# Kernel tuning notes

Hardware: AMD Instinct MI355X
Metric: run time of the kernel (lower is better)

The kernel has to match this reference:

```python
import jax, jax.numpy as jnp
import numpy as np

HIDDEN = 2048
HEADS = 16
HEAD_DIM = HIDDEN // HEADS


def setup_inputs() -> dict:
    key = jax.random.key(0)
    ks = jax.random.split(key, 5)
    scale = 1.0 / np.sqrt(HIDDEN)
    x = jax.random.normal(ks[0], (2, 2048, HIDDEN), dtype=jnp.float32)
    wq = jax.random.normal(ks[1], (HIDDEN, HIDDEN), dtype=jnp.float32) * scale
    wk = jax.random.normal(ks[2], (HIDDEN, HIDDEN), dtype=jnp.float32) * scale
    wv = jax.random.normal(ks[3], (HIDDEN, HIDDEN), dtype=jnp.float32) * scale
    wo = jax.random.normal(ks[4], (HIDDEN, HIDDEN), dtype=jnp.float32) * scale
    return {"x": x, "wq": wq, "wk": wk, "wv": wv, "wo": wo}


def reference(x, wq, wk, wv, wo):
    B, S, D = x.shape
    # nn.Linear(w, bias=False): y = x @ w.T
    q = (x @ wq.T).reshape(B, S, HEADS, HEAD_DIM)
    k = (x @ wk.T).reshape(B, S, HEADS, HEAD_DIM)
    v = (x @ wv.T).reshape(B, S, HEADS, HEAD_DIM)
    scores = jnp.einsum("bqhd,bkhd->bhqk", q, k) / jnp.sqrt(
        jnp.asarray(HEAD_DIM, dtype=x.dtype)
    )
    causal_mask = jnp.triu(jnp.ones((S, S), dtype=bool), k=1)
    scores = jnp.where(causal_mask, -jnp.inf, scores)
    attn = jax.nn.softmax(scores, axis=-1)
    out = jnp.einsum("bhqk,bkhd->bqhd", attn, v).reshape(B, S, D)
    return out @ wo.T
```

## Files before the change

kernel.cpp:

```cpp
#include <hip/hip_runtime.h>
#include <hip/hip_bf16.h>
#include <math.h>

typedef unsigned short u16;
typedef __attribute__((ext_vector_type(8))) short bf16x8;
typedef __attribute__((ext_vector_type(4))) float f32x4;

__device__ static inline u16 f2bf(float f) {
  unsigned u = __float_as_uint(f);
  u += 0x7fff + ((u >> 16) & 1);
  return (u16)(u >> 16);
}

__device__ static inline void gload_lds16(const void* g, void* l) {
  __builtin_amdgcn_global_load_lds(
      (const __attribute__((address_space(1))) unsigned int*)g,
      (__attribute__((address_space(3))) unsigned int*)l, 16, 0, 0);
}

__device__ static inline void store_out(u16* p, float v)   { *p = f2bf(v); }
__device__ static inline void store_out(float* p, float v) { *p = v; }

__global__ void cvt_f32_bf16(const float* __restrict__ src, u16* __restrict__ dst, int n) {
  int stride = gridDim.x * blockDim.x;
  for (int i = blockIdx.x * blockDim.x + threadIdx.x; i * 8 < n; i += stride) {
    const float4* s4 = (const float4*)(src + (size_t)i * 8);
    float4 a = s4[0], b = s4[1];
    u16 t[8] = { f2bf(a.x), f2bf(a.y), f2bf(a.z), f2bf(a.w),
                 f2bf(b.x), f2bf(b.y), f2bf(b.z), f2bf(b.w) };
    *(bf16x8*)(dst + (size_t)i * 8) = *(bf16x8*)t;
  }
}

__global__ void cvt3_f32_bf16(const float* __restrict__ s0, const float* __restrict__ s1,
                              const float* __restrict__ s2, u16* __restrict__ dst) {
  const float* s = blockIdx.y == 0 ? s0 : (blockIdx.y == 1 ? s1 : s2);
  size_t i = ((size_t)blockIdx.x * blockDim.x + threadIdx.x) * 8;
  const float4* s4 = (const float4*)(s + i);
  float4 a = s4[0], b = s4[1];
  u16 t[8] = { f2bf(a.x), f2bf(a.y), f2bf(a.z), f2bf(a.w),
               f2bf(b.x), f2bf(b.y), f2bf(b.z), f2bf(b.w) };
  *(bf16x8*)(dst + (size_t)blockIdx.y * 4194304 + i) = *(bf16x8*)t;
}

template <int NF, typename OutT>
__global__ __launch_bounds__(512, 2)
void gemm2ph(const u16* __restrict__ A, const u16* __restrict__ Bm,
             OutT* __restrict__ C, int M, int N, int K) {
  constexpr int BN = NF * 64;
  __shared__ u16 Abuf[2][256 * 64];
  __shared__ u16 Bbuf[2][BN * 64];
  const int tid = threadIdx.x, lane = tid & 63, w = tid >> 6;
  const int wm = w >> 2, wn = w & 3;
  const int g = lane >> 4, l16 = lane & 15;

  const int per = gridDim.x >> 3;
  const int swz = ((int)blockIdx.x & 7) * per + ((int)blockIdx.x >> 3);
  const int nx = N / BN;
  const int bx = swz % nx, by = swz / nx;
  const int brow = by << 8, bcol = bx * BN;
  const int nt = K >> 6;

  auto stage_Ah = [&](int h, int kt, int d) {
    char* lds = (char*)Abuf[d] + h * 16384;
#pragma unroll
    for (int i = 0; i < 2; ++i) {
      int idx = i * 512 + tid;
      int r = h * 128 + (idx >> 3);
      int c = ((idx & 7) * 16) ^ ((r & 7) << 4);
      gload_lds16((const char*)(A + (size_t)(brow + r) * K + kt * 64) + c,
                  lds + idx * 16);
    }
  };
  auto stage_B = [&](int kt, int d) {
    char* lds = (char*)Bbuf[d];
#pragma unroll
    for (int i = 0; i < NF; ++i) {
      int idx = i * 512 + tid;
      int r = idx >> 3;
      int c = ((idx & 7) * 16) ^ ((r & 7) << 4);
      gload_lds16((const char*)(Bm + (size_t)(bcol + r) * K + kt * 64) + c,
                  lds + idx * 16);
    }
  };

  f32x4 acc[8][NF] = {};
  bf16x8 afr[4][2], bfr[NF][2];

  auto lda = [&](int d, int mf0) {
#pragma unroll
    for (int mf = 0; mf < 4; ++mf) {
      int r = wm * 128 + (mf0 + mf) * 16 + l16;
      const char* base = (const char*)Abuf[d] + r * 128;
      int sw = (r & 7) << 4;
#pragma unroll
      for (int ks = 0; ks < 2; ++ks)
        afr[mf][ks] = *(const bf16x8*)(base + ((ks * 64 + g * 16) ^ sw));
    }
  };
  auto ldb = [&](int d) {
#pragma unroll
    for (int nf = 0; nf < NF; ++nf) {
      int r = wn * (NF * 16) + nf * 16 + l16;
      const char* base = (const char*)Bbuf[d] + r * 128;
      int sw = (r & 7) << 4;
#pragma unroll
      for (int ks = 0; ks < 2; ++ks)
        bfr[nf][ks] = *(const bf16x8*)(base + ((ks * 64 + g * 16) ^ sw));
    }
  };
  auto mma_half = [&](int mf0) {
    __builtin_amdgcn_s_setprio(1);
#pragma unroll
    for (int mf = 0; mf < 4; ++mf)
#pragma unroll
      for (int nf = 0; nf < NF; ++nf)
#pragma unroll
        for (int ks = 0; ks < 2; ++ks)
          acc[mf0 + mf][nf] = __builtin_amdgcn_mfma_f32_16x16x32_bf16(
              afr[mf][ks], bfr[nf][ks], acc[mf0 + mf][nf], 0, 0, 0);
    __builtin_amdgcn_s_setprio(0);
  };

#define WAIT_LGKM() do { \
    asm volatile("s_waitcnt lgkmcnt(0)" ::: "memory"); \
    __builtin_amdgcn_sched_barrier(0); } while (0)
#define WAIT_VM_NF() do { \
    if constexpr (NF == 3) asm volatile("s_waitcnt vmcnt(3)" ::: "memory"); \
    else                   asm volatile("s_waitcnt vmcnt(2)" ::: "memory"); \
    __builtin_amdgcn_sched_barrier(0); } while (0)

  stage_Ah(0, 0, 0); stage_Ah(1, 0, 0);
  stage_B(0, 0);
  stage_B(1, 1);
  WAIT_VM_NF();
  __builtin_amdgcn_s_barrier();

  for (int t = 0; t < nt; ++t) {
    const int cur = t & 1;
    lda(cur, 0); ldb(cur);
    if (t + 1 < nt) stage_Ah(0, t + 1, cur ^ 1);
    __builtin_amdgcn_s_barrier();
    WAIT_LGKM();
    mma_half(0);
    __builtin_amdgcn_s_barrier();
    lda(cur, 4);
    if (t + 1 < nt) stage_Ah(1, t + 1, cur ^ 1);
    if (t + 2 < nt) stage_B(t + 2, cur);
    __builtin_amdgcn_s_barrier();
    WAIT_LGKM();
    mma_half(4);
    if (t + 1 < nt) {
      if (t + 2 < nt) { WAIT_VM_NF(); }
      else {
        asm volatile("s_waitcnt vmcnt(0)" ::: "memory");
        __builtin_amdgcn_sched_barrier(0);
      }
      __builtin_amdgcn_s_barrier();
    }
  }
#undef WAIT_LGKM
#undef WAIT_VM_NF

  const size_t cb = (size_t)(brow + wm * 128) * N + bcol + wn * (NF * 16);
#pragma unroll
  for (int mf = 0; mf < 8; ++mf)
#pragma unroll
    for (int nf = 0; nf < NF; ++nf) {
      int col = nf * 16 + l16;
#pragma unroll
      for (int rr = 0; rr < 4; ++rr) {
        int row = mf * 16 + g * 4 + rr;
        store_out(C + cb + (size_t)row * N + col, acc[mf][nf][rr]);
      }
    }
}

__global__ __launch_bounds__(256)
void transpose_v(const u16* __restrict__ QKV, u16* __restrict__ Vt) {
  __shared__ u16 t[64][72];
  const int tid = threadIdx.x;
  const int b = blockIdx.y >> 5;
  const int s0 = (blockIdx.y & 31) * 64;
  const int hd0 = blockIdx.x * 64;
  const int lr = tid >> 2, lc = (tid & 3) * 16;
  const u16* src = QKV + ((size_t)(b * 2048 + s0 + lr) * 6144 + 4096 + hd0 + lc);
  *(bf16x8*)&t[lr][lc]     = *(const bf16x8*)src;
  *(bf16x8*)&t[lr][lc + 8] = *(const bf16x8*)(src + 8);
  __syncthreads();
  u16 tmp[16];
#pragma unroll
  for (int j = 0; j < 16; ++j) tmp[j] = t[lc + j][lr];
  u16* dst = Vt + ((size_t)(b * 2048 + hd0 + lr) * 2048 + s0 + lc);
  *(bf16x8*)dst       = *(bf16x8*)tmp;
  *(bf16x8*)(dst + 8) = *(bf16x8*)(tmp + 8);
}

__global__ __launch_bounds__(256, 2)
void attn_fwd(const u16* __restrict__ QKV, const u16* __restrict__ Vt,
              u16* __restrict__ AO) {
  __shared__ u16 Ks[2][64 * 128];
  __shared__ u16 Vs[2][128 * 64];
  __shared__ u16 Ps[4][16 * 64];
  const int tid = threadIdx.x, lane = tid & 63, w = tid >> 6;
  const int g = lane >> 4, l16 = lane & 15;
  const int bh = blockIdx.y, b = bh >> 4, h = bh & 15;
  const int fold = blockIdx.x;
  const int pswz = (l16 & 7) << 4;

  for (int phase = 0; phase < 2; ++phase) {
    const int qt = phase == 0 ? fold : 31 - fold;
    const int q0 = qt * 64 + w * 16;

    bf16x8 qf[4];
    {
      const u16* qrow = QKV + ((size_t)(b * 2048 + q0 + l16) * 6144 + h * 128 + g * 8);
#pragma unroll
      for (int c = 0; c < 4; ++c) qf[c] = *(const bf16x8*)(qrow + c * 32);
    }
    f32x4 o[8] = {};
    float mrun = -INFINITY, lrun = 0.f;

    auto stage = [&](int it, int d) {
      int kv0 = it * 64;
#pragma unroll
      for (int i = 0; i < 4; ++i) {
        int idx = i * 256 + tid;
        {
          int row = idx >> 4;
          int scolb = ((idx & 15) * 16) ^ ((row & 7) << 4);
          gload_lds16((const char*)QKV +
                          ((size_t)(b * 2048 + kv0 + row) * 6144 + 2048 + h * 128) * 2 + scolb,
                      (char*)Ks[d] + idx * 16);
        }
        {
          int dd = idx >> 3;
          int vcolb = ((idx & 7) * 16) ^ ((dd & 7) << 4);
          gload_lds16((const char*)Vt + ((size_t)(bh * 128 + dd) * 2048 + kv0) * 2 + vcolb,
                      (char*)Vs[d] + idx * 16);
        }
      }
    };

    const int ntkv = qt + 1;
    stage(0, 0);
    for (int it = 0; it < ntkv; ++it) {
      const int kv0 = it * 64, cur = it & 1;
      if (it + 1 < ntkv) {
        stage(it + 1, cur ^ 1);
        asm volatile("s_waitcnt vmcnt(8)" ::: "memory");
      } else {
        asm volatile("s_waitcnt vmcnt(0)" ::: "memory");
      }
      __builtin_amdgcn_sched_barrier(0);
      __builtin_amdgcn_s_barrier();

      f32x4 s[4];
#pragma unroll
      for (int kb = 0; kb < 4; ++kb) {
        if (kv0 + kb * 16 > q0 + 15) {
          s[kb] = f32x4{-INFINITY, -INFINITY, -INFINITY, -INFINITY};
          continue;
        }
        f32x4 a = {};
        int row = kb * 16 + l16;
        int swzk = (row & 7) << 4;
#pragma unroll
        for (int c = 0; c < 4; ++c) {
          bf16x8 kf = *(const bf16x8*)((const char*)Ks[cur] + row * 256 + ((c * 64 + g * 16) ^ swzk));
          a = __builtin_amdgcn_mfma_f32_16x16x32_bf16(kf, qf[c], a, 0, 0, 0);
        }
        s[kb] = a * 0.08838834764831845f;
      }
      if (kv0 == qt * 64) {
#pragma unroll
        for (int kb = 0; kb < 4; ++kb)
#pragma unroll
          for (int r = 0; r < 4; ++r)
            if (kv0 + kb * 16 + g * 4 + r > q0 + l16) s[kb][r] = -INFINITY;
      }

      float mloc = -INFINITY;
#pragma unroll
      for (int kb = 0; kb < 4; ++kb)
#pragma unroll
        for (int r = 0; r < 4; ++r) mloc = fmaxf(mloc, s[kb][r]);
      mloc = fmaxf(mloc, __shfl_xor(mloc, 16));
      mloc = fmaxf(mloc, __shfl_xor(mloc, 32));
      float mnew = fmaxf(mrun, mloc);
      float al = __expf(mrun - mnew);
      mrun = mnew;
      float rsum = 0.f;
#pragma unroll
      for (int kb = 0; kb < 4; ++kb) {
        float p0 = __expf(s[kb][0] - mnew);
        float p1 = __expf(s[kb][1] - mnew);
        float p2 = __expf(s[kb][2] - mnew);
        float p3 = __expf(s[kb][3] - mnew);
        rsum += (p0 + p1) + (p2 + p3);
        ushort4 pk = { f2bf(p0), f2bf(p1), f2bf(p2), f2bf(p3) };
        *(ushort4*)((char*)Ps[w] + l16 * 128 + ((kb * 32 + g * 8) ^ pswz)) = pk;
      }
      rsum += __shfl_xor(rsum, 16);
      rsum += __shfl_xor(rsum, 32);
      lrun = lrun * al + rsum;

      float alq[4];
#pragma unroll
      for (int r = 0; r < 4; ++r) alq[r] = __shfl(al, g * 4 + r);
#pragma unroll
      for (int db = 0; db < 8; ++db)
#pragma unroll
        for (int r = 0; r < 4; ++r) o[db][r] *= alq[r];

#pragma unroll
      for (int ks = 0; ks < 2; ++ks) {
        if (kv0 + ks * 32 > q0 + 15) continue;
        bf16x8 pa = *(const bf16x8*)((const char*)Ps[w] + l16 * 128 + ((ks * 64 + g * 16) ^ pswz));
#pragma unroll
        for (int db = 0; db < 8; ++db) {
          int row = db * 16 + l16;
          int swzv = (row & 7) << 4;
          bf16x8 vf = *(const bf16x8*)((const char*)Vs[cur] + row * 128 + ((ks * 64 + g * 16) ^ swzv));
          o[db] = __builtin_amdgcn_mfma_f32_16x16x32_bf16(pa, vf, o[db], 0, 0, 0);
        }
      }
      __builtin_amdgcn_s_barrier();
    }

    float rlq[4];
#pragma unroll
    for (int r = 0; r < 4; ++r) rlq[r] = 1.0f / __shfl(lrun, g * 4 + r);
#pragma unroll
    for (int r = 0; r < 4; ++r) {
      int q = q0 + g * 4 + r;
#pragma unroll
      for (int db = 0; db < 8; ++db)
        AO[(size_t)(b * 2048 + q) * 2048 + h * 128 + db * 16 + l16] = f2bf(o[db][r] * rlq[r]);
    }
  }
}

extern "C" void kernel_launch(void* const* d_in, const int* in_sizes, int n_in,
                              void* d_out, int out_size, void* d_ws, size_t ws_size,
                              hipStream_t stream) {
  const float* x  = (const float*)d_in[0];
  const float* wq = (const float*)d_in[1];
  const float* wk = (const float*)d_in[2];
  const float* wv = (const float*)d_in[3];
  const float* wo = (const float*)d_in[4];
  float* out = (float*)d_out;

  char* ws = (char*)d_ws;
  u16* Xb   = (u16*)(ws);
  u16* Wqkv = (u16*)(ws + ((size_t)16 << 20));
  u16* Wob  = (u16*)(ws + ((size_t)40 << 20));
  u16* QKV  = (u16*)(ws + ((size_t)48 << 20));
  u16* Vt   = (u16*)(ws + ((size_t)96 << 20));
  u16* AO   = (u16*)(ws + ((size_t)112 << 20));

  cvt_f32_bf16<<<2048, 256, 0, stream>>>(x, Xb, 2 * 2048 * 2048);
  cvt3_f32_bf16<<<dim3(2048, 3), 256, 0, stream>>>(wq, wk, wv, Wqkv);
  cvt_f32_bf16<<<2048, 256, 0, stream>>>(wo, Wob, 2048 * 2048);

  gemm2ph<3, u16><<<512, 512, 0, stream>>>(Xb, Wqkv, QKV, 4096, 6144, 2048);
  transpose_v<<<dim3(32, 64), 256, 0, stream>>>(QKV, Vt);
  attn_fwd<<<dim3(16, 32), 256, 0, stream>>>(QKV, Vt, AO);
  gemm2ph<2, float><<<256, 512, 0, stream>>>(AO, Wob, out, 4096, 2048, 2048);
}
```

Before: 375.3 us.

## Split GEMM main loop into four phases and add lazy softmax rescaling

The GEMM main loop is split into four MFMA phases by dividing the B fragments into two halves. LDS fragment loads and global-to-LDS staging are interleaved between more barriers, so that data movement overlaps with matrix-core work. In attention, the running max and output rescale are updated only when some lane's max grows by more than a threshold, and fully masked key blocks skip their exp and write zeros. The cost is extra barriers in the GEMM and reliance on fp32 headroom for the deferred rescale.

```diff
diff --git a/kernel.cpp b/kernel.cpp
--- a/kernel.cpp
+++ b/kernel.cpp
@@ -45,9 +45,11 @@
 
 template <int NF, typename OutT>
 __global__ __launch_bounds__(512, 2)
-void gemm2ph(const u16* __restrict__ A, const u16* __restrict__ Bm,
+void gemm4ph(const u16* __restrict__ A, const u16* __restrict__ Bm,
              OutT* __restrict__ C, int M, int N, int K) {
   constexpr int BN = NF * 64;
+  constexpr int NA = (NF + 1) / 2;
+  constexpr int NB = NF - NA;
   __shared__ u16 Abuf[2][256 * 64];
   __shared__ u16 Bbuf[2][BN * 64];
   const int tid = threadIdx.x, lane = tid & 63, w = tid >> 6;
@@ -85,7 +87,7 @@
   };
 
   f32x4 acc[8][NF] = {};
-  bf16x8 afr[4][2], bfr[NF][2];
+  bf16x8 afr[4][2], bfrA[NA][2], bfrB[NB][2];
 
   auto lda = [&](int d, int mf0) {
 #pragma unroll
@@ -98,27 +100,50 @@
         afr[mf][ks] = *(const bf16x8*)(base + ((ks * 64 + g * 16) ^ sw));
     }
   };
-  auto ldb = [&](int d) {
-#pragma unroll
-    for (int nf = 0; nf < NF; ++nf) {
+  auto ldbA = [&](int d) {
+#pragma unroll
+    for (int nf = 0; nf < NA; ++nf) {
       int r = wn * (NF * 16) + nf * 16 + l16;
       const char* base = (const char*)Bbuf[d] + r * 128;
       int sw = (r & 7) << 4;
 #pragma unroll
       for (int ks = 0; ks < 2; ++ks)
-        bfr[nf][ks] = *(const bf16x8*)(base + ((ks * 64 + g * 16) ^ sw));
-    }
-  };
-  auto mma_half = [&](int mf0) {
+        bfrA[nf][ks] = *(const bf16x8*)(base + ((ks * 64 + g * 16) ^ sw));
+    }
+  };
+  auto ldbB = [&](int d) {
+#pragma unroll
+    for (int nf = 0; nf < NB; ++nf) {
+      int r = wn * (NF * 16) + (NA + nf) * 16 + l16;
+      const char* base = (const char*)Bbuf[d] + r * 128;
+      int sw = (r & 7) << 4;
+#pragma unroll
+      for (int ks = 0; ks < 2; ++ks)
+        bfrB[nf][ks] = *(const bf16x8*)(base + ((ks * 64 + g * 16) ^ sw));
+    }
+  };
+  auto mmaA = [&](int mf0) {
     __builtin_amdgcn_s_setprio(1);
 #pragma unroll
     for (int mf = 0; mf < 4; ++mf)
 #pragma unroll
-      for (int nf = 0; nf < NF; ++nf)
+      for (int nf = 0; nf < NA; ++nf)
 #pragma unroll
         for (int ks = 0; ks < 2; ++ks)
           acc[mf0 + mf][nf] = __builtin_amdgcn_mfma_f32_16x16x32_bf16(
-              afr[mf][ks], bfr[nf][ks], acc[mf0 + mf][nf], 0, 0, 0);
+              afr[mf][ks], bfrA[nf][ks], acc[mf0 + mf][nf], 0, 0, 0);
+    __builtin_amdgcn_s_setprio(0);
+  };
+  auto mmaB = [&](int mf0) {
+    __builtin_amdgcn_s_setprio(1);
+#pragma unroll
+    for (int mf = 0; mf < 4; ++mf)
+#pragma unroll
+      for (int nf = 0; nf < NB; ++nf)
+#pragma unroll
+        for (int ks = 0; ks < 2; ++ks)
+          acc[mf0 + mf][NA + nf] = __builtin_amdgcn_mfma_f32_16x16x32_bf16(
+              afr[mf][ks], bfrB[nf][ks], acc[mf0 + mf][NA + nf], 0, 0, 0);
     __builtin_amdgcn_s_setprio(0);
   };
 
@@ -138,18 +163,25 @@
 
   for (int t = 0; t < nt; ++t) {
     const int cur = t & 1;
-    lda(cur, 0); ldb(cur);
+    lda(cur, 0); ldbA(cur);
     if (t + 1 < nt) stage_Ah(0, t + 1, cur ^ 1);
     __builtin_amdgcn_s_barrier();
     WAIT_LGKM();
-    mma_half(0);
+    mmaA(0);
+    __builtin_amdgcn_s_barrier();
+    ldbB(cur);
+    if (t + 1 < nt) stage_Ah(1, t + 1, cur ^ 1);
+    __builtin_amdgcn_s_barrier();
+    WAIT_LGKM();
+    mmaB(0);
     __builtin_amdgcn_s_barrier();
     lda(cur, 4);
-    if (t + 1 < nt) stage_Ah(1, t + 1, cur ^ 1);
     if (t + 2 < nt) stage_B(t + 2, cur);
     __builtin_amdgcn_s_barrier();
     WAIT_LGKM();
-    mma_half(4);
+    mmaB(4);
+    __builtin_amdgcn_s_barrier();
+    mmaA(4);
     if (t + 1 < nt) {
       if (t + 2 < nt) { WAIT_VM_NF(); }
       else {
@@ -288,30 +320,36 @@
       mloc = fmaxf(mloc, __shfl_xor(mloc, 16));
       mloc = fmaxf(mloc, __shfl_xor(mloc, 32));
       float mnew = fmaxf(mrun, mloc);
-      float al = __expf(mrun - mnew);
-      mrun = mnew;
+      if (!__all(mnew - mrun <= 8.f)) {
+        float al = __expf(mrun - mnew);
+        mrun = mnew;
+        lrun *= al;
+        float alq[4];
+#pragma unroll
+        for (int r = 0; r < 4; ++r) alq[r] = __shfl(al, g * 4 + r);
+#pragma unroll
+        for (int db = 0; db < 8; ++db)
+#pragma unroll
+          for (int r = 0; r < 4; ++r) o[db][r] *= alq[r];
+      }
       float rsum = 0.f;
 #pragma unroll
       for (int kb = 0; kb < 4; ++kb) {
-        float p0 = __expf(s[kb][0] - mnew);
-        float p1 = __expf(s[kb][1] - mnew);
-        float p2 = __expf(s[kb][2] - mnew);
-        float p3 = __expf(s[kb][3] - mnew);
+        if (kv0 + kb * 16 > q0 + 15) {
+          *(ushort4*)((char*)Ps[w] + l16 * 128 + ((kb * 32 + g * 8) ^ pswz)) = ushort4{0, 0, 0, 0};
+          continue;
+        }
+        float p0 = __expf(s[kb][0] - mrun);
+        float p1 = __expf(s[kb][1] - mrun);
+        float p2 = __expf(s[kb][2] - mrun);
+        float p3 = __expf(s[kb][3] - mrun);
         rsum += (p0 + p1) + (p2 + p3);
         ushort4 pk = { f2bf(p0), f2bf(p1), f2bf(p2), f2bf(p3) };
         *(ushort4*)((char*)Ps[w] + l16 * 128 + ((kb * 32 + g * 8) ^ pswz)) = pk;
       }
       rsum += __shfl_xor(rsum, 16);
       rsum += __shfl_xor(rsum, 32);
-      lrun = lrun * al + rsum;
-
-      float alq[4];
-#pragma unroll
-      for (int r = 0; r < 4; ++r) alq[r] = __shfl(al, g * 4 + r);
-#pragma unroll
-      for (int db = 0; db < 8; ++db)
-#pragma unroll
-        for (int r = 0; r < 4; ++r) o[db][r] *= alq[r];
+      lrun += rsum;
 
 #pragma unroll
       for (int ks = 0; ks < 2; ++ks) {
@@ -363,8 +401,8 @@
   cvt3_f32_bf16<<<dim3(2048, 3), 256, 0, stream>>>(wq, wk, wv, Wqkv);
   cvt_f32_bf16<<<2048, 256, 0, stream>>>(wo, Wob, 2048 * 2048);
 
-  gemm2ph<3, u16><<<512, 512, 0, stream>>>(Xb, Wqkv, QKV, 4096, 6144, 2048);
+  gemm4ph<3, u16><<<512, 512, 0, stream>>>(Xb, Wqkv, QKV, 4096, 6144, 2048);
   transpose_v<<<dim3(32, 64), 256, 0, stream>>>(QKV, Vt);
   attn_fwd<<<dim3(16, 32), 256, 0, stream>>>(QKV, Vt, AO);
-  gemm2ph<2, float><<<256, 512, 0, stream>>>(AO, Wob, out, 4096, 2048, 2048);
-}
+  gemm4ph<2, float><<<256, 512, 0, stream>>>(AO, Wob, out, 4096, 2048, 2048);
+}
```

Result: slower. 387.8 us (+3.3%).
